# Optimization experiments

Hardware: AMD Instinct MI355X
Metric: run time of the kernel (lower is better)

Reference implementation:

```python
import jax, jax.numpy as jnp
import numpy as np

B, N, K = 128, 512, 6      # graphs, nodes per graph, kNN neighbors
IN_FEAT, POS_DIM, H = 128, 3, 256
NB = B * N                  # total nodes
EPS_BN = 1e-5


def setup_inputs() -> dict:
    key = jax.random.key(0)
    ks = jax.random.split(key, 32)
    inp = {
        "x": jax.random.normal(ks[0], (NB, IN_FEAT), dtype=jnp.float32),
        "pos": jax.random.normal(ks[1], (NB, POS_DIM), dtype=jnp.float32) * 5.0,
    }
    d_in = IN_FEAT + POS_DIM
    def lin(k, fi, fo):
        s = 1.0 / np.sqrt(fi)
        return jax.random.uniform(k, (fi, fo), jnp.float32, -s, s)
    # GCN layers
    inp["W1"] = lin(ks[2], d_in, H); inp["b1"] = jnp.zeros((H,), jnp.float32)
    inp["W2"] = lin(ks[3], H, H);    inp["b2"] = jnp.zeros((H,), jnp.float32)
    inp["W3"] = lin(ks[4], H, H);    inp["b3"] = jnp.zeros((H,), jnp.float32)
    # BatchNorm (eval mode: running stats)
    for i, km, kv in [(1, ks[5], ks[6]), (2, ks[7], ks[8]), (3, ks[9], ks[10])]:
        inp[f"g{i}"]  = jnp.ones((H,), jnp.float32)
        inp[f"be{i}"] = jnp.zeros((H,), jnp.float32)
        inp[f"m{i}"]  = jax.random.normal(km, (H,), jnp.float32) * 0.1
        inp[f"v{i}"]  = jax.random.uniform(kv, (H,), jnp.float32, 0.5, 1.5)
    # attention gate, heads
    inp["gate_w"] = lin(ks[11], H, 1); inp["gate_b"] = jnp.zeros((1,), jnp.float32)
    inp["aff_w"]  = lin(ks[12], H, 1); inp["aff_b"]  = jnp.zeros((1,), jnp.float32)
    inp["rl_w1"]  = lin(ks[13], H, H); inp["rl_b1"]  = jnp.zeros((H,), jnp.float32)
    inp["rl_w2"]  = lin(ks[14], H, POS_DIM); inp["rl_b2"] = jnp.zeros((POS_DIM,), jnp.float32)
    return inp


def _knn_edges(pos):
    # torch_geometric knn_graph semantics: per-graph k nearest neighbors,
    # no self loops, edges (neighbor -> node).  batch = repeat(arange(B), N).
    p = pos.reshape(B, N, POS_DIM)
    sq = jnp.sum(p * p, axis=-1)                                  # [B,N]
    d2 = sq[:, :, None] + sq[:, None, :] - 2.0 * jnp.einsum("bnd,bmd->bnm", p, p)
    d2 = jnp.where(jnp.eye(N, dtype=bool)[None], jnp.inf, d2)     # exclude self
    _, idx = jax.lax.top_k(-d2, K)                                # [B,N,K] local nbr ids
    offs = (jnp.arange(B) * N)[:, None, None]
    src = (idx + offs).reshape(-1)                                # neighbor (source)
    dst = jnp.repeat(jnp.arange(NB), K)                           # target node
    return src, dst


def _gcn(h, W, b, src, dst):
    # GCNConv: add self loops, symmetric norm D^-1/2 (A+I) D^-1/2
    hw = h @ W                                                    # [NB,H]
    deg = jax.ops.segment_sum(jnp.ones_like(dst, jnp.float32), dst, num_segments=NB) + 1.0
    dis = jax.lax.rsqrt(deg)
    norm = dis[src] * dis[dst]                                    # [E]
    agg = jax.ops.segment_sum(hw[src] * norm[:, None], dst, num_segments=NB)
    agg = agg + hw * (1.0 / deg)[:, None]                          # self loop term
    return agg + b


def _bn(h, g, be, m, v):
    return (h - m) * (g * jax.lax.rsqrt(v + EPS_BN)) + be


def reference(x, pos, W1, b1, W2, b2, W3, b3,
              g1, be1, m1, v1, g2, be2, m2, v2, g3, be3, m3, v3,
              gate_w, gate_b, aff_w, aff_b, rl_w1, rl_b1, rl_w2, rl_b2):
    src, dst = _knn_edges(pos)
    h = jnp.concatenate([x, pos], axis=1)                          # [NB, in_feat+3]
    h = jax.nn.relu(_bn(_gcn(h, W1, b1, src, dst), g1, be1, m1, v1))
    h = jax.nn.relu(_bn(_gcn(h, W2, b2, src, dst), g2, be2, m2, v2))
    h = jax.nn.relu(_bn(_gcn(h, W3, b3, src, dst), g3, be3, m3, v3))
    # (dropout is identity in eval mode)
    gate = jax.nn.relu(h @ gate_w + gate_b)[:, 0]                  # [NB]
    attn = jax.nn.softmax(gate.reshape(B, N), axis=1)              # scatter_softmax over batch
    gemb = jnp.einsum("bn,bnh->bh", attn, h.reshape(B, N, H))      # scatter_add of weighted x
    affinity = gemb @ aff_w + aff_b                                # [B,1]
    pose = jax.nn.relu(gemb @ rl_w1 + rl_b1) @ rl_w2 + rl_b2        # [B,3]
    return affinity, pose
```

## Files before the change

### kernel.cpp

```cpp
#include <hip/hip_runtime.h>
#include <hip/hip_bf16.h>
#include <math.h>
#include <float.h>

#define NBG 128
#define NND 512
#define KNN 6
#define NB_TOT (NBG*NND)
#define HF 256
#define NSTEP1 5

typedef short bf16x8 __attribute__((ext_vector_type(8)));
typedef float f32x4 __attribute__((ext_vector_type(4)));

__device__ __forceinline__ int swzoff(int row, int kbyte) {
    return (row*64 + kbyte) ^ (((row>>1)&3)<<4);
}

__device__ __forceinline__ void split_store(const float* v, char* hi_p, char* lo_p) {
    bf16x8 hi, lo;
    #pragma unroll
    for (int j = 0; j < 8; ++j) {
        __hip_bfloat16 h = __float2bfloat16(v[j]);
        float hf = __bfloat162float(h);
        __hip_bfloat16 l = __float2bfloat16(v[j] - hf);
        hi[j] = *(short*)&h;
        lo[j] = *(short*)&l;
    }
    *(bf16x8*)hi_p = hi;
    *(bf16x8*)lo_p = lo;
}

__device__ __forceinline__ int xcd_swz(int bid, int grid) {
    return (bid & 7) * (grid >> 3) + (bid >> 3);
}

__global__ __launch_bounds__(256) void knn_kernel(const float* __restrict__ pos,
                                                  unsigned short* __restrict__ nbr)
{
    const int blk = blockIdx.x;
    const int g = blk >> 3;
    const int chunk = (blk & 7) * 64;
    const int tid = threadIdx.x;
    const int node = chunk + (tid >> 2);
    const int sub = tid & 3;

    __shared__ float4 p4[NND + (NND>>6)];
    const float* pg = pos + (size_t)g * NND * 3;
    for (int n = tid; n < NND; n += 256) {
        float x = pg[n*3+0], y = pg[n*3+1], z = pg[n*3+2];
        p4[n + (n>>6)] = make_float4(x, y, z, x*x + y*y + z*z);
    }
    __syncthreads();

    const float4 pi = p4[node + (node>>6)];
    const float m2x = -2.0f*pi.x, m2y = -2.0f*pi.y, m2z = -2.0f*pi.z;

    float bdA[KNN], bdB[KNN]; int biA[KNN], biB[KNN];
    #pragma unroll
    for (int q = 0; q < KNN; ++q) {
        bdA[q] = FLT_MAX; biA[q] = 0x7fffffff;
        bdB[q] = FLT_MAX; biB[q] = 0x7fffffff;
    }

    const int j0 = sub * 128;
    const float4* baseA = &p4[sub*130];
    const float4* baseB = &p4[sub*130 + 65];

    #pragma unroll 2
    for (int t = 0; t < 64; ++t) {
        int ja = j0 + t, jb = j0 + 64 + t;
        float4 pa = baseA[t];
        float4 pb = baseB[t];
        float da = fmaf(m2z, pa.z, fmaf(m2y, pa.y, fmaf(m2x, pa.x, pa.w)));
        float db = fmaf(m2z, pb.z, fmaf(m2y, pb.y, fmaf(m2x, pb.x, pb.w)));
        da = (ja == node) ? FLT_MAX : da;
        db = (jb == node) ? FLT_MAX : db;
        float ca = da; int ia = ja;
        float cb = db; int ib = jb;
        #pragma unroll
        for (int q = 0; q < KNN; ++q) {
            bool sa = ca < bdA[q];
            float t1 = sa ? ca : bdA[q]; float t2 = sa ? bdA[q] : ca;
            int   t3 = sa ? ia : biA[q]; int   t4 = sa ? biA[q] : ia;
            bdA[q] = t1; ca = t2; biA[q] = t3; ia = t4;
            bool sb = cb < bdB[q];
            float u1 = sb ? cb : bdB[q]; float u2 = sb ? bdB[q] : cb;
            int   u3 = sb ? ib : biB[q]; int   u4 = sb ? biB[q] : ib;
            bdB[q] = u1; cb = u2; biB[q] = u3; ib = u4;
        }
    }

    float ld[KNN]; int li[KNN];
    #pragma unroll
    for (int q = 0; q < KNN; ++q) {
        float ad = bdA[q], xd = bdB[KNN-1-q];
        int   ai = biA[q], xi = biB[KNN-1-q];
        bool t = (ad < xd) || (ad == xd && ai < xi);
        ld[q] = t ? ad : xd;
        li[q] = t ? ai : xi;
    }
    #pragma unroll
    for (int pass = 0; pass < KNN-1; ++pass)
        #pragma unroll
        for (int a = 0; a < KNN-1-pass; ++a) {
            int b = a+1;
            bool sw = (ld[b] < ld[a]) || (ld[b] == ld[a] && li[b] < li[a]);
            float td = sw ? ld[b] : ld[a]; float ud = sw ? ld[a] : ld[b];
            int   ti = sw ? li[b] : li[a]; int   ui = sw ? li[a] : li[b];
            ld[a] = td; li[a] = ti; ld[b] = ud; li[b] = ui;
        }

    #pragma unroll
    for (int mi = 0; mi < 2; ++mi) {
        const int mask = 1 << mi;
        float od[KNN]; int oi[KNN];
        #pragma unroll
        for (int q = 0; q < KNN; ++q) {
            od[q] = __shfl_xor(ld[q], mask);
            oi[q] = __shfl_xor(li[q], mask);
        }
        #pragma unroll
        for (int q = 0; q < KNN; ++q) {
            float ad = ld[q], xd = od[KNN-1-q];
            int   ai = li[q], xi = oi[KNN-1-q];
            bool t = (ad < xd) || (ad == xd && ai < xi);
            ld[q] = t ? ad : xd;
            li[q] = t ? ai : xi;
        }
        #pragma unroll
        for (int pass = 0; pass < KNN-1; ++pass)
            #pragma unroll
            for (int a = 0; a < KNN-1-pass; ++a) {
                int b = a+1;
                bool sw = (ld[b] < ld[a]) || (ld[b] == ld[a] && li[b] < li[a]);
                float td = sw ? ld[b] : ld[a]; float ud = sw ? ld[a] : ld[b];
                int   ti = sw ? li[b] : li[a]; int   ui = sw ? li[a] : li[b];
                ld[a] = td; li[a] = ti; ld[b] = ud; li[b] = ui;
            }
    }

    if (sub == 0) {
        int base = (g*NND + node)*KNN;
        #pragma unroll
        for (int q = 0; q < KNN; ++q) nbr[base+q] = (unsigned short)li[q];
    }
}

__global__ __launch_bounds__(256) void prew_all(
    const float* __restrict__ W1, const float* __restrict__ W2,
    const float* __restrict__ W3,
    char* __restrict__ I1, char* __restrict__ I2, char* __restrict__ I3)
{
    int b = blockIdx.x;
    const float* W; char* img; int K, nstep;
    if (b < 20)      { W = W1; img = I1; K = 131; nstep = 5; }
    else if (b < 52) { W = W2; img = I2; K = 256; nstep = 8; b -= 20; }
    else             { W = W3; img = I3; K = 256; nstep = 8; b -= 52; }
    int gid = b*256 + threadIdx.x;
    int per_nb = nstep*512;
    int nb = gid / per_nb;
    int r  = gid - nb*per_nb;
    int step = r >> 9;
    int r2 = r & 511;
    int cl = r2 >> 2;
    int kc = (r2 & 3) * 8;
    float v[8];
    #pragma unroll
    for (int j = 0; j < 8; ++j) {
        int gk = step*32 + kc + j;
        v[j] = (gk < K) ? W[(size_t)gk*256 + nb*128 + cl] : 0.f;
    }
    char* base = img + (size_t)nb*nstep*16384 + (size_t)step*16384;
    int off = swzoff(cl, kc*2);
    split_store(v, base + off, base + 8192 + off);
}

__global__ __launch_bounds__(256) void agg_first(const float* __restrict__ x,
                                                 const float* __restrict__ pos,
                                                 const unsigned short* __restrict__ nbr,
                                                 char* __restrict__ Aimg)
{
    int gid = xcd_swz(blockIdx.x, gridDim.x)*256 + threadIdx.x;
    int i = gid / 20, ch = gid - i*20;
    const float rs = 1.0f/sqrtf(7.0f);
    const float c1 = rs*rs, c2 = 1.0f/7.0f;
    const int gbase = i & ~(NND-1);
    float v[8];
    if (ch < 16) {
        int jn[KNN];
        #pragma unroll
        for (int q = 0; q < KNN; ++q) jn[q] = gbase + nbr[i*KNN+q];
        const float4* x4 = (const float4*)x;
        int c4 = ch*2;
        float4 s0 = x4[(size_t)i*32 + c4], s1 = x4[(size_t)i*32 + c4 + 1];
        float a0=0,a1=0,a2=0,a3=0,b0=0,b1=0,b2=0,b3=0;
        #pragma unroll
        for (int q = 0; q < KNN; ++q) {
            float4 t0 = x4[(size_t)jn[q]*32 + c4];
            float4 t1 = x4[(size_t)jn[q]*32 + c4 + 1];
            a0+=t0.x; a1+=t0.y; a2+=t0.z; a3+=t0.w;
            b0+=t1.x; b1+=t1.y; b2+=t1.z; b3+=t1.w;
        }
        v[0]=a0*c1+s0.x*c2; v[1]=a1*c1+s0.y*c2; v[2]=a2*c1+s0.z*c2; v[3]=a3*c1+s0.w*c2;
        v[4]=b0*c1+s1.x*c2; v[5]=b1*c1+s1.y*c2; v[6]=b2*c1+s1.z*c2; v[7]=b3*c1+s1.w*c2;
    } else if (ch == 16) {
        int jn[KNN];
        #pragma unroll
        for (int q = 0; q < KNN; ++q) jn[q] = gbase + nbr[i*KNN+q];
        float ax=0, ay=0, az=0;
        #pragma unroll
        for (int q = 0; q < KNN; ++q) {
            ax += pos[(size_t)jn[q]*3+0];
            ay += pos[(size_t)jn[q]*3+1];
            az += pos[(size_t)jn[q]*3+2];
        }
        v[0] = ax*c1 + pos[(size_t)i*3+0]*c2;
        v[1] = ay*c1 + pos[(size_t)i*3+1]*c2;
        v[2] = az*c1 + pos[(size_t)i*3+2]*c2;
        v[3]=v[4]=v[5]=v[6]=v[7]=0.f;
    } else {
        #pragma unroll
        for (int j = 0; j < 8; ++j) v[j] = 0.f;
    }
    int mb = i >> 7, row = i & 127, step = ch >> 2, kbyte = (ch & 3)*16;
    char* base = Aimg + (size_t)mb*(NSTEP1*16384) + (size_t)step*16384;
    int off = swzoff(row, kbyte);
    split_store(v, base + off, base + 8192 + off);
}

__global__ __launch_bounds__(256,4) void gemm_mfma(
    const char* __restrict__ Aimg, const char* __restrict__ Wimg, int nstep,
    const float* __restrict__ bias,
    const float* __restrict__ gam, const float* __restrict__ bet,
    const float* __restrict__ mu,  const float* __restrict__ var,
    float* __restrict__ out)
{
    __shared__ uint4 lds4[34816/16];
    char* lds  = (char*)lds4;
    char* Alds = lds;
    char* Wlds = lds + 16384;
    float* scs = (float*)(lds + 32768);
    float* shs = scs + 256;
    const int tid = threadIdx.x;
    const int lane = tid & 63, wave = tid >> 6;
    const int wm = wave >> 1, wn = wave & 1;
    const int mblk = blockIdx.x, nblk = blockIdx.y;

    if (tid < 256) {
        float s = gam[tid] / sqrtf(var[tid] + 1e-5f);
        scs[tid] = s;
        shs[tid] = bet[tid] + (bias[tid] - mu[tid]) * s;
    }

    const char* Ab = Aimg + (size_t)mblk * nstep * 16384;
    const char* Wb = Wimg + (size_t)nblk * nstep * 16384;

    const char* gbase; char* lbase;
    int soff;
    if (wave < 2) { gbase = Ab;  lbase = Alds; soff = wave*8192; }
    else          { gbase = Wb;  lbase = Wlds; soff = (wave-2)*8192; }

    f32x4 acc[4][4];
    #pragma unroll
    for (int m = 0; m < 4; ++m)
        #pragma unroll
        for (int n = 0; n < 4; ++n) acc[m][n] = (f32x4){0.f,0.f,0.f,0.f};

    for (int s = 0; s < nstep; ++s) {
        #pragma unroll
        for (int i = 0; i < 8; ++i) {
            int off = soff + i*1024;
            __builtin_amdgcn_global_load_lds(
                (const __attribute__((address_space(1))) void*)(gbase + (size_t)s*16384 + off + lane*16),
                (__attribute__((address_space(3))) void*)(lbase + off), 16, 0, 0);
        }
        __syncthreads();
        const int kb = (lane >> 4) * 16;
        bf16x8 ah[4], al[4];
        #pragma unroll
        for (int m = 0; m < 4; ++m) {
            int row = wm*64 + m*16 + (lane & 15);
            int off = swzoff(row, kb);
            ah[m] = *(const bf16x8*)(Alds + off);
            al[m] = *(const bf16x8*)(Alds + 8192 + off);
        }
        #pragma unroll
        for (int n = 0; n < 4; ++n) {
            int col = wn*64 + n*16 + (lane & 15);
            int off = swzoff(col, kb);
            bf16x8 bh = *(const bf16x8*)(Wlds + off);
            bf16x8 bl = *(const bf16x8*)(Wlds + 8192 + off);
            #pragma unroll
            for (int m = 0; m < 4; ++m) {
                acc[m][n] = __builtin_amdgcn_mfma_f32_16x16x32_bf16(ah[m], bh, acc[m][n], 0, 0, 0);
                acc[m][n] = __builtin_amdgcn_mfma_f32_16x16x32_bf16(al[m], bh, acc[m][n], 0, 0, 0);
                acc[m][n] = __builtin_amdgcn_mfma_f32_16x16x32_bf16(ah[m], bl, acc[m][n], 0, 0, 0);
            }
        }
        __syncthreads();
    }

    #pragma unroll
    for (int n = 0; n < 4; ++n) {
        int c = nblk*128 + wn*64 + n*16 + (lane & 15);
        float sc = scs[c], sh = shs[c];
        #pragma unroll
        for (int m = 0; m < 4; ++m) {
            int r0 = mblk*128 + wm*64 + m*16 + (lane >> 4)*4;
            #pragma unroll
            for (int q = 0; q < 4; ++q) {
                float v = acc[m][n][q]*sc + sh;
                out[(size_t)(r0+q)*256 + c] = fmaxf(v, 0.f);
            }
        }
    }
}

__global__ __launch_bounds__(512,2) void gcn_fused(
    const float* __restrict__ hin,
    const unsigned short* __restrict__ nbr,
    const char* __restrict__ Wimg,
    const float* __restrict__ bias,
    const float* __restrict__ gam, const float* __restrict__ bet,
    const float* __restrict__ mu,  const float* __restrict__ var,
    float* __restrict__ hout)
{
    __shared__ uint4 lds4[51200/16];
    char* Alds = (char*)lds4;
    char* Wlds = (char*)lds4 + 16384;
    float* scs = (float*)((char*)lds4 + 49152);
    float* shs = scs + 256;
    const int tid = threadIdx.x;
    const int lane = tid & 63, wave = tid >> 6;
    const int wm = wave >> 2, wn = wave & 3;
    const int mblk = xcd_swz(blockIdx.x, gridDim.x);

    if (tid < 256) {
        float s = gam[tid] / sqrtf(var[tid] + 1e-5f);
        scs[tid] = s;
        shs[tid] = bet[tid] + (bias[tid] - mu[tid]) * s;
    }

    const int arow = tid >> 2, ch = tid & 3;
    const int gnode = mblk*128 + arow;
    const int gb = gnode & ~(NND-1);
    int jn[KNN];
    #pragma unroll
    for (int q = 0; q < KNN; ++q) jn[q] = gb + nbr[gnode*KNN + q];
    const float rs = 1.0f/sqrtf(7.0f);
    const float c1 = rs*rs, c2 = 1.0f/7.0f;
    const int aoff = swzoff(arow, ch*16);
    const float4* h4 = (const float4*)hin;

    f32x4 acc[4][4];
    #pragma unroll
    for (int m = 0; m < 4; ++m)
        #pragma unroll
        for (int n = 0; n < 4; ++n) acc[m][n] = (f32x4){0.f,0.f,0.f,0.f};

    for (int s = 0; s < 8; ++s) {
        #pragma unroll
        for (int i = 0; i < 4; ++i) {
            int woff = i*8192 + wave*1024;
            size_t srcoff = (i < 2) ? ((size_t)s*16384 + woff)
                                    : ((size_t)(8+s)*16384 + (woff - 16384));
            __builtin_amdgcn_global_load_lds(
                (const __attribute__((address_space(1))) void*)(Wimg + srcoff + lane*16),
                (__attribute__((address_space(3))) void*)(Wlds + woff), 16, 0, 0);
        }
        {
            const int fb = s*8 + ch*2;
            float a0=0,a1=0,a2=0,a3=0,b0=0,b1=0,b2=0,b3=0;
            #pragma unroll
            for (int q = 0; q < KNN; ++q) {
                float4 t0 = h4[(size_t)jn[q]*64 + fb];
                float4 t1 = h4[(size_t)jn[q]*64 + fb + 1];
                a0+=t0.x; a1+=t0.y; a2+=t0.z; a3+=t0.w;
                b0+=t1.x; b1+=t1.y; b2+=t1.z; b3+=t1.w;
            }
            float4 s0 = h4[(size_t)gnode*64 + fb];
            float4 s1 = h4[(size_t)gnode*64 + fb + 1];
            float v[8];
            v[0]=a0*c1+s0.x*c2; v[1]=a1*c1+s0.y*c2; v[2]=a2*c1+s0.z*c2; v[3]=a3*c1+s0.w*c2;
            v[4]=b0*c1+s1.x*c2; v[5]=b1*c1+s1.y*c2; v[6]=b2*c1+s1.z*c2; v[7]=b3*c1+s1.w*c2;
            split_store(v, Alds + aoff, Alds + 8192 + aoff);
        }
        __syncthreads();
        const int kb = (lane >> 4) * 16;
        bf16x8 ah[4], al[4];
        #pragma unroll
        for (int m = 0; m < 4; ++m) {
            int r = wm*64 + m*16 + (lane & 15);
            int o = swzoff(r, kb);
            ah[m] = *(const bf16x8*)(Alds + o);
            al[m] = *(const bf16x8*)(Alds + 8192 + o);
        }
        const char* wreg = Wlds + ((wn >= 2) ? 16384 : 0);
        #pragma unroll
        for (int n = 0; n < 4; ++n) {
            int cl = (wn & 1)*64 + n*16 + (lane & 15);
            int o = swzoff(cl, kb);
            bf16x8 bh = *(const bf16x8*)(wreg + o);
            bf16x8 bl = *(const bf16x8*)(wreg + 8192 + o);
            #pragma unroll
            for (int m = 0; m < 4; ++m) {
                acc[m][n] = __builtin_amdgcn_mfma_f32_16x16x32_bf16(ah[m], bh, acc[m][n], 0, 0, 0);
                acc[m][n] = __builtin_amdgcn_mfma_f32_16x16x32_bf16(al[m], bh, acc[m][n], 0, 0, 0);
                acc[m][n] = __builtin_amdgcn_mfma_f32_16x16x32_bf16(ah[m], bl, acc[m][n], 0, 0, 0);
            }
        }
        __syncthreads();
    }

    #pragma unroll
    for (int n = 0; n < 4; ++n) {
        int c = wn*64 + n*16 + (lane & 15);
        float sc = scs[c], sh = shs[c];
        #pragma unroll
        for (int m = 0; m < 4; ++m) {
            int r0 = mblk*128 + wm*64 + m*16 + (lane >> 4)*4;
            #pragma unroll
            for (int q = 0; q < 4; ++q) {
                float v = acc[m][n][q]*sc + sh;
                hout[(size_t)(r0+q)*256 + c] = fmaxf(v, 0.f);
            }
        }
    }
}

__global__ __launch_bounds__(256) void gate_kernel(const float* __restrict__ h3,
                                                   const float* __restrict__ gate_w,
                                                   const float* __restrict__ gate_b,
                                                   float* __restrict__ gate)
{
    const int lane = threadIdx.x & 63;
    const int gw = (blockIdx.x*256 + threadIdx.x) >> 6;
    float4 w4 = ((const float4*)gate_w)[lane];
    float gb = gate_b[0];
    #pragma unroll
    for (int it = 0; it < 4; ++it) {
        int r = gw + it*8192;
        float4 v = ((const float4*)(h3 + (size_t)r*HF))[lane];
        float s = v.x*w4.x + v.y*w4.y + v.z*w4.z + v.w*w4.w;
        #pragma unroll
        for (int o = 32; o > 0; o >>= 1) s += __shfl_xor(s, o, 64);
        if (lane == 0) gate[r] = fmaxf(s + gb, 0.f);
    }
}

__device__ __forceinline__ float blk_sum256(float v, volatile float* red)
{
    #pragma unroll
    for (int o = 32; o > 0; o >>= 1) v += __shfl_xor(v, o, 64);
    __syncthreads();
    if ((threadIdx.x & 63) == 0) red[threadIdx.x >> 6] = v;
    __syncthreads();
    return (red[0] + red[1]) + (red[2] + red[3]);
}

__global__ __launch_bounds__(256) void gemb_kernel(const float* __restrict__ h3,
                                                   const float* __restrict__ gate,
                                                   float* __restrict__ gembp)
{
    const int g = blockIdx.x, s = blockIdx.y;
    const int tid = threadIdx.x, lane = tid & 63, w = tid >> 6;
    __shared__ float at[128];
    __shared__ float red4[4][HF];
    __shared__ float red[4];

    float g0 = gate[g*NND + tid];
    float g1 = gate[g*NND + 256 + tid];
    float m = fmaxf(g0, g1);
    #pragma unroll
    for (int o = 32; o > 0; o >>= 1) m = fmaxf(m, __shfl_xor(m, o, 64));
    if ((tid & 63) == 0) red[tid >> 6] = m;
    __syncthreads();
    m = fmaxf(fmaxf(red[0], red[1]), fmaxf(red[2], red[3]));
    float S = blk_sum256(expf(g0 - m) + expf(g1 - m), red);
    if (tid < 128) at[tid] = expf(gate[g*NND + s*128 + tid] - m) / S;
    __syncthreads();

    const float* hb = h3 + (size_t)(g*NND + s*128 + w*32) * HF;
    float4 acc = make_float4(0.f, 0.f, 0.f, 0.f);
    #pragma unroll 4
    for (int n = 0; n < 32; ++n) {
        float a = at[w*32 + n];
        float4 v = ((const float4*)(hb + (size_t)n*HF))[lane];
        acc.x = fmaf(a, v.x, acc.x); acc.y = fmaf(a, v.y, acc.y);
        acc.z = fmaf(a, v.z, acc.z); acc.w = fmaf(a, v.w, acc.w);
    }
    *(float4*)&red4[w][lane*4] = acc;
    __syncthreads();
    if (tid < HF) {
        float sum = (red4[0][tid] + red4[1][tid]) + (red4[2][tid] + red4[3][tid]);
        gembp[((size_t)s*NBG + g)*HF + tid] = sum;
    }
}

__global__ __launch_bounds__(256) void heads_kernel(
    const float* __restrict__ gembp,
    const float* __restrict__ aff_w,  const float* __restrict__ aff_b,
    const float* __restrict__ rl_w1,  const float* __restrict__ rl_b1,
    const float* __restrict__ rl_w2,  const float* __restrict__ rl_b2,
    float* __restrict__ out)
{
    int g = blockIdx.x, tid = threadIdx.x;
    __shared__ float gemb[HF];
    __shared__ float red[4];
    float acc = (gembp[((size_t)0*NBG + g)*HF + tid] + gembp[((size_t)1*NBG + g)*HF + tid])
              + (gembp[((size_t)2*NBG + g)*HF + tid] + gembp[((size_t)3*NBG + g)*HF + tid]);
    gemb[tid] = acc;
    __syncthreads();

    float sa = blk_sum256(acc * aff_w[tid], red);
    if (tid == 0) out[g] = sa + aff_b[0];

    float t = rl_b1[tid];
    #pragma unroll 4
    for (int k2 = 0; k2 < HF; ++k2)
        t = fmaf(gemb[k2], rl_w1[(size_t)k2*HF + tid], t);
    t = fmaxf(t, 0.f);
    float s0 = blk_sum256(t * rl_w2[(size_t)tid*3 + 0], red);
    if (tid == 0) out[128 + g*3 + 0] = s0 + rl_b2[0];
    float s1 = blk_sum256(t * rl_w2[(size_t)tid*3 + 1], red);
    if (tid == 0) out[128 + g*3 + 1] = s1 + rl_b2[1];
    float s2 = blk_sum256(t * rl_w2[(size_t)tid*3 + 2], red);
    if (tid == 0) out[128 + g*3 + 2] = s2 + rl_b2[2];
}

extern "C" void kernel_launch(void* const* d_in, const int* in_sizes, int n_in,
                              void* d_out, int out_size, void* d_ws, size_t ws_size,
                              hipStream_t stream)
{
    const float* x      = (const float*)d_in[0];
    const float* pos    = (const float*)d_in[1];
    const float* W1     = (const float*)d_in[2];
    const float* b1     = (const float*)d_in[3];
    const float* W2     = (const float*)d_in[4];
    const float* b2     = (const float*)d_in[5];
    const float* W3     = (const float*)d_in[6];
    const float* b3     = (const float*)d_in[7];
    const float* g1     = (const float*)d_in[8];
    const float* be1    = (const float*)d_in[9];
    const float* m1     = (const float*)d_in[10];
    const float* v1     = (const float*)d_in[11];
    const float* g2     = (const float*)d_in[12];
    const float* be2    = (const float*)d_in[13];
    const float* m2     = (const float*)d_in[14];
    const float* v2     = (const float*)d_in[15];
    const float* g3     = (const float*)d_in[16];
    const float* be3    = (const float*)d_in[17];
    const float* m3     = (const float*)d_in[18];
    const float* v3     = (const float*)d_in[19];
    const float* gate_w = (const float*)d_in[20];
    const float* gate_b = (const float*)d_in[21];
    const float* aff_w  = (const float*)d_in[22];
    const float* aff_b  = (const float*)d_in[23];
    const float* rl_w1  = (const float*)d_in[24];
    const float* rl_b1  = (const float*)d_in[25];
    const float* rl_w2  = (const float*)d_in[26];
    const float* rl_b2  = (const float*)d_in[27];
    float* out = (float*)d_out;

    char* wsb = (char*)d_ws;
    unsigned short* nbr = (unsigned short*)wsb;
    char* Wimg1 = wsb + 786432;
    char* Wimg2 = Wimg1 + (size_t)2*NSTEP1*16384;
    char* Wimg3 = Wimg2 + (size_t)2*8*16384;
    float* h_a  = (float*)(Wimg3 + (size_t)2*8*16384);
    char* regB  = (char*)(h_a + (size_t)NB_TOT*HF);
    char*  Aimg  = regB;
    float* h_b   = (float*)regB;
    float* gate  = (float*)regB;
    float* gembp = (float*)(regB + (size_t)NB_TOT*4);

    knn_kernel<<<NBG*8, 256, 0, stream>>>(pos, nbr);
    prew_all<<<84, 256, 0, stream>>>(W1, W2, W3, Wimg1, Wimg2, Wimg3);

    agg_first<<<(NB_TOT*20)/256, 256, 0, stream>>>(x, pos, nbr, Aimg);
    gemm_mfma<<<dim3(NB_TOT/128, 2), 256, 0, stream>>>(Aimg, Wimg1, NSTEP1,
        b1, g1, be1, m1, v1, h_a);
    gcn_fused<<<NB_TOT/128, 512, 0, stream>>>(h_a, nbr, Wimg2,
        b2, g2, be2, m2, v2, h_b);
    gcn_fused<<<NB_TOT/128, 512, 0, stream>>>(h_b, nbr, Wimg3,
        b3, g3, be3, m3, v3, h_a);

    gate_kernel<<<2048, 256, 0, stream>>>(h_a, gate_w, gate_b, gate);
    gemb_kernel<<<dim3(NBG, 4), 256, 0, stream>>>(h_a, gate, gembp);
    heads_kernel<<<NBG, 256, 0, stream>>>(gembp, aff_w, aff_b,
                                          rl_w1, rl_b1, rl_w2, rl_b2, out);
}
```

Measured before the change: 229.8 us.

## Shrink fused GCN tile to 64 rows and prefetch neighbor gathers into registers

```diff
diff --git a/kernel.cpp b/kernel.cpp
--- a/kernel.cpp
+++ b/kernel.cpp
@@ -317,7 +317,7 @@
     }
 }
 
-__global__ __launch_bounds__(512,2) void gcn_fused(
+__global__ __launch_bounds__(256,3) void gcn_fused(
     const float* __restrict__ hin,
     const unsigned short* __restrict__ nbr,
     const char* __restrict__ Wimg,
@@ -326,24 +326,24 @@
     const float* __restrict__ mu,  const float* __restrict__ var,
     float* __restrict__ hout)
 {
-    __shared__ uint4 lds4[51200/16];
+    __shared__ uint4 lds4[43008/16];
     char* Alds = (char*)lds4;
-    char* Wlds = (char*)lds4 + 16384;
-    float* scs = (float*)((char*)lds4 + 49152);
+    char* Wlds = (char*)lds4 + 8192;
+    float* scs = (float*)((char*)lds4 + 40960);
     float* shs = scs + 256;
     const int tid = threadIdx.x;
     const int lane = tid & 63, wave = tid >> 6;
-    const int wm = wave >> 2, wn = wave & 3;
+    const int wn = wave;
     const int mblk = xcd_swz(blockIdx.x, gridDim.x);
 
-    if (tid < 256) {
+    {
         float s = gam[tid] / sqrtf(var[tid] + 1e-5f);
         scs[tid] = s;
         shs[tid] = bet[tid] + (bias[tid] - mu[tid]) * s;
     }
 
     const int arow = tid >> 2, ch = tid & 3;
-    const int gnode = mblk*128 + arow;
+    const int gnode = mblk*64 + arow;
     const int gb = gnode & ~(NND-1);
     int jn[KNN];
     #pragma unroll
@@ -359,44 +359,64 @@
         #pragma unroll
         for (int n = 0; n < 4; ++n) acc[m][n] = (f32x4){0.f,0.f,0.f,0.f};
 
+    float4 pf[14];
+    {
+        const int fb = ch*2;
+        #pragma unroll
+        for (int q = 0; q < KNN; ++q) {
+            pf[2*q]   = h4[(size_t)jn[q]*64 + fb];
+            pf[2*q+1] = h4[(size_t)jn[q]*64 + fb + 1];
+        }
+        pf[12] = h4[(size_t)gnode*64 + fb];
+        pf[13] = h4[(size_t)gnode*64 + fb + 1];
+    }
+
     for (int s = 0; s < 8; ++s) {
-        #pragma unroll
-        for (int i = 0; i < 4; ++i) {
-            int woff = i*8192 + wave*1024;
-            size_t srcoff = (i < 2) ? ((size_t)s*16384 + woff)
-                                    : ((size_t)(8+s)*16384 + (woff - 16384));
+        {
+            float a0 = pf[0].x + pf[2].x + pf[4].x + pf[6].x + pf[8].x + pf[10].x;
+            float a1 = pf[0].y + pf[2].y + pf[4].y + pf[6].y + pf[8].y + pf[10].y;
+            float a2 = pf[0].z + pf[2].z + pf[4].z + pf[6].z + pf[8].z + pf[10].z;
+            float a3 = pf[0].w + pf[2].w + pf[4].w + pf[6].w + pf[8].w + pf[10].w;
+            float b0 = pf[1].x + pf[3].x + pf[5].x + pf[7].x + pf[9].x + pf[11].x;
+            float b1 = pf[1].y + pf[3].y + pf[5].y + pf[7].y + pf[9].y + pf[11].y;
+            float b2 = pf[1].z + pf[3].z + pf[5].z + pf[7].z + pf[9].z + pf[11].z;
+            float b3 = pf[1].w + pf[3].w + pf[5].w + pf[7].w + pf[9].w + pf[11].w;
+            float v[8];
+            v[0]=a0*c1+pf[12].x*c2; v[1]=a1*c1+pf[12].y*c2;
+            v[2]=a2*c1+pf[12].z*c2; v[3]=a3*c1+pf[12].w*c2;
+            v[4]=b0*c1+pf[13].x*c2; v[5]=b1*c1+pf[13].y*c2;
+            v[6]=b2*c1+pf[13].z*c2; v[7]=b3*c1+pf[13].w*c2;
+            split_store(v, Alds + aoff, Alds + 4096 + aoff);
+        }
+        #pragma unroll
+        for (int i = 0; i < 8; ++i) {
+            int woff = i*4096 + wave*1024;
+            size_t srcoff = (woff < 16384) ? ((size_t)s*16384 + woff)
+                                           : ((size_t)(8+s)*16384 + (woff - 16384));
             __builtin_amdgcn_global_load_lds(
                 (const __attribute__((address_space(1))) void*)(Wimg + srcoff + lane*16),
                 (__attribute__((address_space(3))) void*)(Wlds + woff), 16, 0, 0);
         }
-        {
-            const int fb = s*8 + ch*2;
-            float a0=0,a1=0,a2=0,a3=0,b0=0,b1=0,b2=0,b3=0;
+        __syncthreads();
+        if (s < 7) {
+            const int fb = (s+1)*8 + ch*2;
             #pragma unroll
             for (int q = 0; q < KNN; ++q) {
-                float4 t0 = h4[(size_t)jn[q]*64 + fb];
-                float4 t1 = h4[(size_t)jn[q]*64 + fb + 1];
-                a0+=t0.x; a1+=t0.y; a2+=t0.z; a3+=t0.w;
-                b0+=t1.x; b1+=t1.y; b2+=t1.z; b3+=t1.w;
+                pf[2*q]   = h4[(size_t)jn[q]*64 + fb];
+                pf[2*q+1] = h4[(size_t)jn[q]*64 + fb + 1];
             }
-            float4 s0 = h4[(size_t)gnode*64 + fb];
-            float4 s1 = h4[(size_t)gnode*64 + fb + 1];
-            float v[8];
-            v[0]=a0*c1+s0.x*c2; v[1]=a1*c1+s0.y*c2; v[2]=a2*c1+s0.z*c2; v[3]=a3*c1+s0.w*c2;
-            v[4]=b0*c1+s1.x*c2; v[5]=b1*c1+s1.y*c2; v[6]=b2*c1+s1.z*c2; v[7]=b3*c1+s1.w*c2;
-            split_store(v, Alds + aoff, Alds + 8192 + aoff);
-        }
-        __syncthreads();
+            pf[12] = h4[(size_t)gnode*64 + fb];
+            pf[13] = h4[(size_t)gnode*64 + fb + 1];
+        }
         const int kb = (lane >> 4) * 16;
         bf16x8 ah[4], al[4];
         #pragma unroll
         for (int m = 0; m < 4; ++m) {
-            int r = wm*64 + m*16 + (lane & 15);
-            int o = swzoff(r, kb);
+            int o = swzoff(m*16 + (lane & 15), kb);
             ah[m] = *(const bf16x8*)(Alds + o);
-            al[m] = *(const bf16x8*)(Alds + 8192 + o);
-        }
-        const char* wreg = Wlds + ((wn >= 2) ? 16384 : 0);
+            al[m] = *(const bf16x8*)(Alds + 4096 + o);
+        }
+        const char* wreg = Wlds + (wn >> 1)*16384;
         #pragma unroll
         for (int n = 0; n < 4; ++n) {
             int cl = (wn & 1)*64 + n*16 + (lane & 15);
@@ -419,7 +439,7 @@
         float sc = scs[c], sh = shs[c];
         #pragma unroll
         for (int m = 0; m < 4; ++m) {
-            int r0 = mblk*128 + wm*64 + m*16 + (lane >> 4)*4;
+            int r0 = mblk*64 + m*16 + (lane >> 4)*4;
             #pragma unroll
             for (int q = 0; q < 4; ++q) {
                 float v = acc[m][n][q]*sc + sh;
@@ -581,9 +601,9 @@
     agg_first<<<(NB_TOT*20)/256, 256, 0, stream>>>(x, pos, nbr, Aimg);
     gemm_mfma<<<dim3(NB_TOT/128, 2), 256, 0, stream>>>(Aimg, Wimg1, NSTEP1,
         b1, g1, be1, m1, v1, h_a);
-    gcn_fused<<<NB_TOT/128, 512, 0, stream>>>(h_a, nbr, Wimg2,
+    gcn_fused<<<NB_TOT/64, 256, 0, stream>>>(h_a, nbr, Wimg2,
         b2, g2, be2, m2, v2, h_b);
-    gcn_fused<<<NB_TOT/128, 512, 0, stream>>>(h_b, nbr, Wimg3,
+    gcn_fused<<<NB_TOT/64, 256, 0, stream>>>(h_b, nbr, Wimg3,
         b3, g3, be3, m3, v3, h_a);
 
     gate_kernel<<<2048, 256, 0, stream>>>(h_a, gate_w, gate_b, gate);
```

Result: faster. 215.2 us (-6.4%).
